# Performance work log

Hardware: AMD Instinct MI355X
Metric: run time of the kernel (lower is better)

Reference implementation:

```python
import jax, jax.numpy as jnp
import numpy as np

D_Z, D_Y, N, N_SAMPLE = 512, 32, 2048, 128
JITTER = 0.0001


def setup_inputs() -> dict:
    key = jax.random.key(0)
    k1, k2, k3, k4, k5 = jax.random.split(key, 5)
    d_total = D_Z + N * D_Y
    return {
        "m": jax.random.normal(k1, (d_total,), jnp.float32),
        "Lz": jax.random.normal(k2, (D_Z, D_Z), jnp.float32),
        "Ly_blocks": jax.random.normal(k3, (N, D_Y, D_Y), jnp.float32),
        "Lyz": jax.random.normal(k4, (N * D_Y, D_Z), jnp.float32),
        "eps": jax.random.normal(k5, (N_SAMPLE, d_total), jnp.float32),
    }


def reference(m, Lz, Ly_blocks, Lyz, eps):
    # L_dense (block lower-triangular) is never materialized; we compute
    # z = m + eps @ L_dense.T block-wise. L_dense = [[tril(Lz), 0], [Lyz, blkdiag(tril(Ly_n))]] + jitter*I.
    dt = Lz.dtype
    Lz_t = jnp.tril(Lz) + JITTER * jnp.eye(D_Z, dtype=dt)
    Ly = jnp.tril(Ly_blocks) + JITTER * jnp.eye(D_Y, dtype=dt)  # [N, d_y, d_y]

    eps_z = eps[:, :D_Z]                          # [S, d_z]
    eps_y = eps[:, D_Z:].reshape(-1, N, D_Y)      # [S, N, d_y]

    z_z = m[:D_Z] + eps_z @ Lz_t.T                # [S, d_z]
    cross = eps_z @ Lyz.T                         # [S, N*d_y]
    diag = jnp.einsum("snj,nij->sni", eps_y, Ly).reshape(-1, N * D_Y)
    z_y = m[D_Z:] + cross + diag                  # [S, N*d_y]
    return jnp.concatenate([z_z, z_y], axis=1)
```

## Files before the change

kernel.cpp:

```cpp
#include <hip/hip_runtime.h>

#define DZ 512
#define DT 66048
#define NTILE 2064
#define SV_JITTER 1e-4f

typedef __attribute__((ext_vector_type(8))) short bf8;
typedef __attribute__((ext_vector_type(4))) short bf4;
typedef __attribute__((ext_vector_type(4))) float f4;

__device__ __forceinline__ short f2bf(float f) {
  unsigned u = __builtin_bit_cast(unsigned, f);
  return (short)((u + 0x7FFFu + ((u >> 16) & 1u)) >> 16);
}

__device__ __forceinline__ bf8 cvt8(float4 a, float4 b) {
  bf8 r = { f2bf(a.x), f2bf(a.y), f2bf(a.z), f2bf(a.w),
            f2bf(b.x), f2bf(b.y), f2bf(b.z), f2bf(b.w) };
  return r;
}

__device__ __forceinline__ bf8 cvt8_tril(float4 x, float4 y, int kbase, int diag) {
  float v[8] = {x.x, x.y, x.z, x.w, y.x, y.y, y.z, y.w};
  bf8 r;
  #pragma unroll
  for (int t = 0; t < 8; ++t) {
    int k = kbase + t;
    float val = (k < diag) ? v[t] : ((k == diag) ? v[t] + SV_JITTER : 0.f);
    r[t] = f2bf(val);
  }
  return r;
}

__global__ __launch_bounds__(512, 2)
void sv_kernel(const float* __restrict__ mv, const float* __restrict__ Lz,
               const float* __restrict__ Ly, const float* __restrict__ Lyz,
               const float* __restrict__ eps, float* __restrict__ out) {
  __shared__ short Afrag[128 * 512];
  __shared__ short Bpan[32 * 512];

  const int tid = threadIdx.x;
  const int lane = tid & 63;
  const int wv = tid >> 6;
  const int lcol = lane & 15;
  const int q = lane >> 4;
  const int b = blockIdx.x;

  float4 sv[8];
  auto stage_load = [&](int T) {
    const float* Ls = (T < 16) ? (Lz + (size_t)(32 * T) * DZ)
                               : (Lyz + (size_t)(32 * T - DZ) * DZ);
    #pragma unroll
    for (int i = 0; i < 8; ++i)
      sv[i] = *(const float4*)(Ls + (size_t)4 * (i * 512 + tid));
  };
  auto stage_write = [&](int T) {
    #pragma unroll
    for (int i = 0; i < 8; ++i) {
      const int f = i * 512 + tid;
      const int ro = f >> 7;
      const int c4 = f & 127;
      const float v[4] = {sv[i].x, sv[i].y, sv[i].z, sv[i].w};
      bf4 w;
      if (T < 16) {
        const int gcol = 32 * T + ro;
        #pragma unroll
        for (int t = 0; t < 4; ++t) {
          const int k = 4 * c4 + t;
          const float val =
              (k < gcol) ? v[t] : ((k == gcol) ? v[t] + SV_JITTER : 0.f);
          w[t] = f2bf(val);
        }
      } else {
        #pragma unroll
        for (int t = 0; t < 4; ++t) w[t] = f2bf(v[t]);
      }
      const int off = (ro << 10) + ((((c4 >> 1) ^ (ro & 7))) << 4) + ((c4 & 1) << 3);
      *(bf4*)((char*)Bpan + off) = w;
    }
  };
  auto readB = [&](int g, int kk) -> bf8 {
    const int R = 16 * g + lcol;
    const int off = (R << 10) + (((4 * kk + q) ^ (R & 7)) << 4);
    return *(const bf8*)((const char*)Bpan + off);
  };

  stage_load(b);
  {
    const int slot = lane;
    const int r0 = wv * 16;
    #pragma unroll 4
    for (int i = 0; i < 16; ++i) {
      const int r = r0 + i;
      const float* p = eps + (size_t)(16 * (r & 7) + (slot & 15)) * DT +
                       (r >> 3) * 32 + (slot >> 4) * 8;
      const float4 x = *(const float4*)p;
      const float4 y = *(const float4*)(p + 4);
      *(bf8*)&Afrag[r * 512 + slot * 8] = cvt8(x, y);
    }
  }
  stage_write(b);
  __syncthreads();

  #pragma unroll 1
  for (int r = 0; r < 9; ++r) {
    const int T = r * 256 + b;
    if (T >= NTILE) break;
    const bool isz = (T < 16);
    const int Tn = T + 256;
    const bool have_next = (Tn < NTILE);

    if (have_next) stage_load(Tn);

    float4 dax, day, db0x, db0y, db1x, db1y;
    if (!isz) {
      const int nb = T - 16;
      const float* pa =
          eps + (size_t)(16 * wv + lcol) * DT + DZ + (size_t)nb * 32 + 8 * q;
      dax = *(const float4*)pa; day = *(const float4*)(pa + 4);
      const float* pb0 = Ly + ((size_t)nb * 32 + lcol) * 32 + 8 * q;
      db0x = *(const float4*)pb0; db0y = *(const float4*)(pb0 + 4);
      const float* pb1 = Ly + ((size_t)nb * 32 + 16 + lcol) * 32 + 8 * q;
      db1x = *(const float4*)pb1; db1y = *(const float4*)(pb1 + 4);
    }

    f4 acc0 = f4{0.f, 0.f, 0.f, 0.f};
    f4 acc1 = f4{0.f, 0.f, 0.f, 0.f};
    #pragma unroll
    for (int kk = 0; kk < 16; ++kk) {
      const bf8 af = *(const bf8*)&Afrag[(kk * 8 + wv) * 512 + lane * 8];
      const bf8 b0 = readB(0, kk);
      const bf8 b1 = readB(1, kk);
      acc0 = __builtin_amdgcn_mfma_f32_16x16x32_bf16(af, b0, acc0, 0, 0, 0);
      acc1 = __builtin_amdgcn_mfma_f32_16x16x32_bf16(af, b1, acc1, 0, 0, 0);
    }
    if (!isz) {
      const bf8 afd = cvt8(dax, day);
      const bf8 dbf0 = cvt8_tril(db0x, db0y, 8 * q, lcol);
      const bf8 dbf1 = cvt8_tril(db1x, db1y, 8 * q, 16 + lcol);
      acc0 = __builtin_amdgcn_mfma_f32_16x16x32_bf16(afd, dbf0, acc0, 0, 0, 0);
      acc1 = __builtin_amdgcn_mfma_f32_16x16x32_bf16(afd, dbf1, acc1, 0, 0, 0);
    }

    {
      const int c0 = 32 * T + lcol;
      const float m0 = mv[c0], m1 = mv[c0 + 16];
      #pragma unroll
      for (int rr = 0; rr < 4; ++rr) {
        const size_t rowoff = (size_t)(16 * wv + 4 * q + rr) * DT;
        out[rowoff + c0] = acc0[rr] + m0;
        out[rowoff + c0 + 16] = acc1[rr] + m1;
      }
    }

    __syncthreads();
    if (have_next) stage_write(Tn);
    __syncthreads();
  }
}

extern "C" void kernel_launch(void* const* d_in, const int* in_sizes, int n_in,
                              void* d_out, int out_size, void* d_ws, size_t ws_size,
                              hipStream_t stream) {
  const float* m   = (const float*)d_in[0];
  const float* Lz  = (const float*)d_in[1];
  const float* Ly  = (const float*)d_in[2];
  const float* Lyz = (const float*)d_in[3];
  const float* eps = (const float*)d_in[4];
  float* out = (float*)d_out;
  sv_kernel<<<dim3(256), dim3(512), 0, stream>>>(m, Lz, Ly, Lyz, eps, out);
}
```

Before: 50.83 us.

## Double-buffer half-width B panels and transpose MFMA for vectorized output stores

Splits each 32-column output tile into two 16-column half tiles, stages them through a double-buffered LDS panel, and prefetches the next-next panel and the next diagonal block into registers. This drops one of the two barriers per iteration. The MFMA operands are swapped so each lane holds four consecutive output columns, allowing float4 stores of the output and float4 loads of m instead of scalar accesses. In exchange each block runs twice as many iterations with half the MFMA work per iteration, which may raise loop and barrier overhead per unit of compute.

New measurement: 55.45 us. 1.09x slower.

```diff
diff --git a/kernel.cpp b/kernel.cpp
--- a/kernel.cpp
+++ b/kernel.cpp
@@ -2,7 +2,7 @@
 
 #define DZ 512
 #define DT 66048
-#define NTILE 2064
+#define NH 4128
 #define SV_JITTER 1e-4f
 
 typedef __attribute__((ext_vector_type(8))) short bf8;
@@ -37,7 +37,7 @@
                const float* __restrict__ Ly, const float* __restrict__ Lyz,
                const float* __restrict__ eps, float* __restrict__ out) {
   __shared__ short Afrag[128 * 512];
-  __shared__ short Bpan[32 * 512];
+  __shared__ short Bh[2][16 * 512];
 
   const int tid = threadIdx.x;
   const int lane = tid & 63;
@@ -46,24 +46,24 @@
   const int q = lane >> 4;
   const int b = blockIdx.x;
 
-  float4 sv[8];
-  auto stage_load = [&](int T) {
-    const float* Ls = (T < 16) ? (Lz + (size_t)(32 * T) * DZ)
-                               : (Lyz + (size_t)(32 * T - DZ) * DZ);
+  float4 sv[4];
+  auto sissue = [&](int h) {
+    const float* Ls = (h < 32) ? (Lz + (size_t)(16 * h) * DZ)
+                               : (Lyz + (size_t)(16 * h) * DZ - (size_t)DZ * DZ);
     #pragma unroll
-    for (int i = 0; i < 8; ++i)
+    for (int i = 0; i < 4; ++i)
       sv[i] = *(const float4*)(Ls + (size_t)4 * (i * 512 + tid));
   };
-  auto stage_write = [&](int T) {
+  auto swrite = [&](int h, short* buf) {
     #pragma unroll
-    for (int i = 0; i < 8; ++i) {
+    for (int i = 0; i < 4; ++i) {
       const int f = i * 512 + tid;
       const int ro = f >> 7;
       const int c4 = f & 127;
       const float v[4] = {sv[i].x, sv[i].y, sv[i].z, sv[i].w};
       bf4 w;
-      if (T < 16) {
-        const int gcol = 32 * T + ro;
+      if (h < 32) {
+        const int gcol = 16 * h + ro;
         #pragma unroll
         for (int t = 0; t < 4; ++t) {
           const int k = 4 * c4 + t;
@@ -76,16 +76,26 @@
         for (int t = 0; t < 4; ++t) w[t] = f2bf(v[t]);
       }
       const int off = (ro << 10) + ((((c4 >> 1) ^ (ro & 7))) << 4) + ((c4 & 1) << 3);
-      *(bf4*)((char*)Bpan + off) = w;
+      *(bf4*)((char*)buf + off) = w;
     }
   };
-  auto readB = [&](int g, int kk) -> bf8 {
-    const int R = 16 * g + lcol;
-    const int off = (R << 10) + (((4 * kk + q) ^ (R & 7)) << 4);
-    return *(const bf8*)((const char*)Bpan + off);
+  auto readB = [&](const short* buf, int kk) -> bf8 {
+    const int off = (lcol << 10) + ((((kk << 2) + q) ^ (lcol & 7)) << 4);
+    return *(const bf8*)((const char*)buf + off);
+  };
+  auto diag_load = [&](int h, float4& ax, float4& ay, float4& bx, float4& by) {
+    const int nb = (16 * h - DZ) >> 5;
+    const int i0 = (16 * h) & 16;
+    const float* pa =
+        eps + (size_t)(16 * wv + lcol) * DT + DZ + (size_t)nb * 32 + 8 * q;
+    ax = *(const float4*)pa; ay = *(const float4*)(pa + 4);
+    const float* pb = Ly + ((size_t)nb * 32 + i0 + lcol) * 32 + 8 * q;
+    bx = *(const float4*)pb; by = *(const float4*)(pb + 4);
   };
 
-  stage_load(b);
+  const int nh = (b < 32) ? 17 : 16;
+
+  sissue(b);
   {
     const int slot = lane;
     const int r0 = wv * 16;
@@ -99,62 +109,48 @@
       *(bf8*)&Afrag[r * 512 + slot * 8] = cvt8(x, y);
     }
   }
-  stage_write(b);
+  swrite(b, Bh[0]);
+  if (nh > 1) sissue(b + 256);
+  float4 cdax{}, cday{}, cdbx{}, cdby{};
+  if (b >= 32) diag_load(b, cdax, cday, cdbx, cdby);
   __syncthreads();
 
   #pragma unroll 1
-  for (int r = 0; r < 9; ++r) {
-    const int T = r * 256 + b;
-    if (T >= NTILE) break;
-    const bool isz = (T < 16);
-    const int Tn = T + 256;
-    const bool have_next = (Tn < NTILE);
+  for (int j = 0; j < 17; ++j) {
+    if (j >= nh) break;
+    const int h = b + 256 * j;
+    const bool isz = (h < 32);
 
-    if (have_next) stage_load(Tn);
+    if (j + 1 < nh) swrite(b + 256 * (j + 1), Bh[(j + 1) & 1]);
+    if (j + 2 < nh) sissue(b + 256 * (j + 2));
+    float4 ndax{}, nday{}, ndbx{}, ndby{};
+    if (j + 1 < nh) diag_load(b + 256 * (j + 1), ndax, nday, ndbx, ndby);
 
-    float4 dax, day, db0x, db0y, db1x, db1y;
-    if (!isz) {
-      const int nb = T - 16;
-      const float* pa =
-          eps + (size_t)(16 * wv + lcol) * DT + DZ + (size_t)nb * 32 + 8 * q;
-      dax = *(const float4*)pa; day = *(const float4*)(pa + 4);
-      const float* pb0 = Ly + ((size_t)nb * 32 + lcol) * 32 + 8 * q;
-      db0x = *(const float4*)pb0; db0y = *(const float4*)(pb0 + 4);
-      const float* pb1 = Ly + ((size_t)nb * 32 + 16 + lcol) * 32 + 8 * q;
-      db1x = *(const float4*)pb1; db1y = *(const float4*)(pb1 + 4);
-    }
-
-    f4 acc0 = f4{0.f, 0.f, 0.f, 0.f};
-    f4 acc1 = f4{0.f, 0.f, 0.f, 0.f};
+    const short* buf = Bh[j & 1];
+    f4 acc = f4{0.f, 0.f, 0.f, 0.f};
     #pragma unroll
     for (int kk = 0; kk < 16; ++kk) {
       const bf8 af = *(const bf8*)&Afrag[(kk * 8 + wv) * 512 + lane * 8];
-      const bf8 b0 = readB(0, kk);
-      const bf8 b1 = readB(1, kk);
-      acc0 = __builtin_amdgcn_mfma_f32_16x16x32_bf16(af, b0, acc0, 0, 0, 0);
-      acc1 = __builtin_amdgcn_mfma_f32_16x16x32_bf16(af, b1, acc1, 0, 0, 0);
+      const bf8 bf = readB(buf, kk);
+      acc = __builtin_amdgcn_mfma_f32_16x16x32_bf16(bf, af, acc, 0, 0, 0);
     }
     if (!isz) {
-      const bf8 afd = cvt8(dax, day);
-      const bf8 dbf0 = cvt8_tril(db0x, db0y, 8 * q, lcol);
-      const bf8 dbf1 = cvt8_tril(db1x, db1y, 8 * q, 16 + lcol);
-      acc0 = __builtin_amdgcn_mfma_f32_16x16x32_bf16(afd, dbf0, acc0, 0, 0, 0);
-      acc1 = __builtin_amdgcn_mfma_f32_16x16x32_bf16(afd, dbf1, acc1, 0, 0, 0);
+      const bf8 afd = cvt8(cdax, cday);
+      const int i0 = (16 * h) & 16;
+      const bf8 dbf = cvt8_tril(cdbx, cdby, 8 * q, i0 + lcol);
+      acc = __builtin_amdgcn_mfma_f32_16x16x32_bf16(dbf, afd, acc, 0, 0, 0);
     }
 
     {
-      const int c0 = 32 * T + lcol;
-      const float m0 = mv[c0], m1 = mv[c0 + 16];
-      #pragma unroll
-      for (int rr = 0; rr < 4; ++rr) {
-        const size_t rowoff = (size_t)(16 * wv + 4 * q + rr) * DT;
-        out[rowoff + c0] = acc0[rr] + m0;
-        out[rowoff + c0 + 16] = acc1[rr] + m1;
-      }
+      const int c0 = 16 * h + 4 * q;
+      const float4 m4 = *(const float4*)(mv + c0);
+      float4 o;
+      o.x = acc[0] + m4.x; o.y = acc[1] + m4.y;
+      o.z = acc[2] + m4.z; o.w = acc[3] + m4.w;
+      *(float4*)(out + (size_t)(16 * wv + lcol) * DT + c0) = o;
     }
 
-    __syncthreads();
-    if (have_next) stage_write(Tn);
+    cdax = ndax; cday = nday; cdbx = ndbx; cdby = ndby;
     __syncthreads();
   }
 }
```
